# Optimization experiments

Hardware: AMD Instinct MI355X
Metric: run time of the kernel (lower is better)

Reference implementation:

```python
import jax, jax.numpy as jnp
import numpy as np

EMBED_DIM = 1024
NUM_HEADS = 16
HEAD_DIM = EMBED_DIM // NUM_HEADS


def setup_inputs() -> dict:
    key = jax.random.key(0)
    ks = jax.random.split(key, 9)
    B, S, D = 2, 2048, EMBED_DIM
    scale = 1.0 / np.sqrt(D)
    x = jax.random.normal(ks[0], (B, S, D), dtype=jnp.float32)
    # Linear params (torch nn.Linear: y = x @ W.T + b); store W as [out, in]
    Wq = jax.random.normal(ks[1], (D, D), dtype=jnp.float32) * scale
    bq = jnp.zeros((D,), dtype=jnp.float32)
    Wk = jax.random.normal(ks[2], (D, D), dtype=jnp.float32) * scale
    bk = jnp.zeros((D,), dtype=jnp.float32)
    Wv = jax.random.normal(ks[3], (D, D), dtype=jnp.float32) * scale
    bv = jnp.zeros((D,), dtype=jnp.float32)
    Wo = jax.random.normal(ks[4], (D, D), dtype=jnp.float32) * scale
    bo = jnp.zeros((D,), dtype=jnp.float32)
    return {"x": x, "Wq": Wq, "bq": bq, "Wk": Wk, "bk": bk,
            "Wv": Wv, "bv": bv, "Wo": Wo, "bo": bo}


def reference(x, Wq, bq, Wk, bk, Wv, bv, Wo, bo):
    B, S, D = x.shape
    H, Hd = NUM_HEADS, HEAD_DIM
    scaling = Hd ** -0.5
    # projections (torch Linear: x @ W.T + b)
    q = (x @ Wq.T + bq).reshape(B, S, H, Hd).transpose(0, 2, 1, 3)  # [B,H,S,Hd]
    k = (x @ Wk.T + bk).reshape(B, S, H, Hd).transpose(0, 2, 1, 3)
    v = (x @ Wv.T + bv).reshape(B, S, H, Hd).transpose(0, 2, 1, 3)
    # full score matrix, as in the original (no flash tiling)
    scores = jnp.einsum('bhqd,bhkd->bhqk', q, k) * scaling  # [B,H,S,S]
    attn = jax.nn.softmax(scores, axis=-1)
    # dropout is identity in eval mode
    out = jnp.einsum('bhqk,bhkd->bhqd', attn, v)  # [B,H,S,Hd]
    out = out.transpose(0, 2, 1, 3).reshape(B, S, D)
    return out @ Wo.T + bo
```

## Files before the change

kernel.cpp:

```cpp
#include <hip/hip_runtime.h>
#include <stdint.h>

typedef unsigned short u16;
typedef short short8 __attribute__((ext_vector_type(8)));
typedef short bh4 __attribute__((ext_vector_type(4)));
typedef float f32x4 __attribute__((ext_vector_type(4)));

__device__ __forceinline__ u16 f2bf_fast(float f) {
  union { float f; uint32_t u; } x;
  x.f = f;
  return (u16)((x.u + 0x8000u) >> 16);
}

__device__ __forceinline__ uint32_t pack2bf(float lo, float hi) {
  union { float f; uint32_t u; } a, b;
  a.f = lo; b.f = hi;
  return __builtin_amdgcn_perm(b.u + 0x8000u, a.u + 0x8000u, 0x07060302u);
}

__device__ __forceinline__ float bf2f(uint32_t u) {
  union { uint32_t u; float f; } x;
  x.u = u << 16;
  return x.f;
}

__device__ __forceinline__ void gload_lds16(const void* g, void* l) {
  __builtin_amdgcn_global_load_lds(
      (const __attribute__((address_space(1))) void*)g,
      (__attribute__((address_space(3))) void*)l, 16, 0, 0);
}

__device__ __forceinline__ f32x4 mfma16(short8 a, short8 b, f32x4 c) {
  return __builtin_amdgcn_mfma_f32_16x16x32_bf16(a, b, c, 0, 0, 0);
}

__device__ __forceinline__ f32x4 pv_mfma(bh4 a, bh4 b, f32x4 c) {
#if defined(__AMDGCN__) || defined(__HIP_DEVICE_COMPILE__)
  return __builtin_amdgcn_mfma_f32_16x16x16bf16_1k(a, b, c, 0, 0, 0);
#else
  (void)a; (void)b;
  return c;
#endif
}

__device__ __forceinline__ short8 ldfrag(const u16* base, int tile, int kc,
                                         int lane) {
  return *(const short8*)(base + ((((tile << 5) + kc) << 6) + lane) * 8);
}

#define QSCALE 0.18033688011112042f

__global__ void pack_all(const float* __restrict__ x, const float* __restrict__ wq,
                         const float* __restrict__ wk, const float* __restrict__ wv,
                         const float* __restrict__ wo, u16* __restrict__ xp,
                         u16* __restrict__ wp) {
  const int gi = blockIdx.x * 256 + threadIdx.x;
  const int lane = gi & 63;
  const int kc = (gi >> 6) & 31;
  const int rt = gi >> 11;
  const int col = kc * 32 + (lane >> 4) * 8;
  const float* src;
  int row;
  if (rt < 256) {
    src = x;
    row = rt * 16 + (lane & 15);
  } else {
    const int wti = rt - 256;
    const int widx = wti >> 6;
    src = (widx == 0) ? wq : (widx == 1) ? wk : (widx == 2) ? wv : wo;
    row = (wti & 63) * 16 + (lane & 15);
  }
  const float4* p = (const float4*)(src + (size_t)row * 1024 + col);
  const float4 v0 = p[0], v1 = p[1];
  uint4 o;
  o.x = pack2bf(v0.x, v0.y);
  o.y = pack2bf(v0.z, v0.w);
  o.z = pack2bf(v1.x, v1.y);
  o.w = pack2bf(v1.z, v1.w);
  u16* dst = (rt < 256) ? xp : wp;
  const int og = (rt < 256) ? gi : gi - 524288;
  ((uint4*)dst)[og] = o;
}

__global__ __launch_bounds__(256, 3) void proj_qkv(
    const u16* __restrict__ xp, const u16* __restrict__ wp,
    const float* __restrict__ bq, const float* __restrict__ bk,
    const float* __restrict__ bv, u16* __restrict__ qw, u16* __restrict__ kw,
    u16* __restrict__ vw) {
  const int gid = blockIdx.x * 4 + (threadIdx.x >> 6);
  const int lane = threadIdx.x & 63;
  const int quad = lane >> 4, l15 = lane & 15;
  const bool isQK = gid < 2048;
  int at0, bt0, bm, bn;
  const u16 *Ap, *Bp;
  if (isQK) {
    bn = gid >> 6; bm = gid & 63;
    Ap = xp; at0 = bm * 4;
    Bp = wp; bt0 = bn * 4;
  } else {
    const int h = gid - 2048;
    bn = h & 63; bm = h >> 6;
    Ap = wp; at0 = 128 + bm * 4;
    Bp = xp; bt0 = bn * 4;
  }

  f32x4 acc[4][4] = {};
  short8 af[2][4], bf[2][4];
#pragma unroll
  for (int mt = 0; mt < 4; ++mt) af[0][mt] = ldfrag(Ap, at0 + mt, 0, lane);
#pragma unroll
  for (int nt = 0; nt < 4; ++nt) bf[0][nt] = ldfrag(Bp, bt0 + nt, 0, lane);

#pragma unroll 4
  for (int kc = 0; kc < 32; ++kc) {
    const int cur = kc & 1, nxt = cur ^ 1;
    if (kc < 31) {
#pragma unroll
      for (int mt = 0; mt < 4; ++mt)
        af[nxt][mt] = ldfrag(Ap, at0 + mt, kc + 1, lane);
#pragma unroll
      for (int nt = 0; nt < 4; ++nt)
        bf[nxt][nt] = ldfrag(Bp, bt0 + nt, kc + 1, lane);
    }
#pragma unroll
    for (int mt = 0; mt < 4; ++mt)
#pragma unroll
      for (int nt = 0; nt < 4; ++nt)
        acc[mt][nt] = mfma16(af[cur][mt], bf[cur][nt], acc[mt][nt]);
  }

#pragma unroll
  for (int nt = 0; nt < 4; ++nt) {
    const int n = bn * 64 + nt * 16 + l15;
#pragma unroll
    for (int mt = 0; mt < 4; ++mt)
#pragma unroll
      for (int r = 0; r < 4; ++r) {
        const int m = bm * 64 + mt * 16 + quad * 4 + r;
        const float a = acc[mt][nt][r];
        if (isQK) {
          const bool isQ = (bn < 16);
          const int nn = isQ ? n : n - 1024;
          const float v = isQ ? (a + bq[nn]) * QSCALE : a + bk[nn];
          u16* op = isQ ? qw : kw;
          const int b = m >> 11, s = m & 2047, hh = nn >> 6, d = nn & 63;
          op[((size_t)((b * 16 + hh) * 2048 + s)) * 64 + d] = f2bf_fast(v);
        } else {
          const float v = a + bv[m];
          const int b = n >> 11, s = n & 2047;
          vw[((size_t)(b * 1024 + m)) * 2048 + s] = f2bf_fast(v);
        }
      }
  }
}

__global__ __launch_bounds__(256) void attn_kernel(
    const u16* __restrict__ Q, const u16* __restrict__ Kt,
    const u16* __restrict__ Vt, u16* __restrict__ op0, u16* __restrict__ op1,
    float* __restrict__ lp) {
  __shared__ __align__(16) u16 Sm[16384];
  const int tid = threadIdx.x, lane = tid & 63, w = tid >> 6;
  const int quad = lane >> 4, l15 = lane & 15;
  const int qt = blockIdx.x;
  const int bh = blockIdx.y >> 1;
  const int ks = blockIdx.y & 1;

  const char* Qb = (const char*)(Q + ((size_t)bh * 2048 + qt * 128) * 64);
  const char* Kb = (const char*)(Kt + ((size_t)bh * 2048 + ks * 1024) * 64);
  const char* Vb = (const char*)(Vt + (size_t)bh * 64 * 2048 + ks * 1024);

  auto stageKV = [&](int kt, int b) {
    u16* Kl = Sm + b * 4096;
    u16* Vl = Sm + 8192 + b * 4096;
#pragma unroll
    for (int i = 0; i < 2; ++i) {
      const int G = (w * 2 + i) * 64 + lane;
      const int r = G >> 3, sl = G & 7;
      gload_lds16(Kb + (size_t)(kt * 64 + r) * 128 + ((sl ^ (r & 7)) * 16),
                  &Kl[G * 8]);
      gload_lds16(Vb + (size_t)r * 4096 + kt * 128 + ((sl ^ (r & 7)) * 16),
                  &Vl[G * 8]);
    }
  };

#pragma unroll
  for (int i = 0; i < 4; ++i) {
    const int G = (w * 4 + i) * 64 + lane;
    const int row = G >> 3, sl = G & 7;
    u16* qdst = (G < 512) ? (Sm + 4096) : (Sm + 12288);
    gload_lds16(Qb + (size_t)row * 128 + ((sl ^ (row & 7)) * 16),
                &qdst[(G & 511) * 8]);
  }
  stageKV(0, 0);
  __syncthreads();

  const u16* qreg = (w < 2) ? (Sm + 4096) : (Sm + 12288);
  const int qr0 = (w & 1) * 32;
  short8 aq[2][2];
#pragma unroll
  for (int mt = 0; mt < 2; ++mt)
#pragma unroll
    for (int kc = 0; kc < 2; ++kc)
      aq[mt][kc] = *(const short8*)&qreg[(qr0 + mt * 16 + l15) * 64 +
                                         (((kc * 4 + quad) ^ (l15 & 7)) * 8)];
  __syncthreads();

  f32x4 ot[4][2] = {};
  float lsum[2] = {};

  for (int kt = 0; kt < 16; ++kt) {
    const int buf = kt & 1;
    if (kt < 15) stageKV(kt + 1, buf ^ 1);
    const u16* Kl = Sm + buf * 4096;
    const u16* Vl = Sm + 8192 + buf * 4096;

    f32x4 st[2][4] = {};
#pragma unroll
    for (int kc = 0; kc < 2; ++kc)
#pragma unroll
      for (int ntk = 0; ntk < 4; ++ntk) {
        short8 kf = *(const short8*)&Kl[(ntk * 16 + l15) * 64 +
                                        (((kc * 4 + quad) ^ (l15 & 7)) * 8)];
        st[0][ntk] = mfma16(kf, aq[0][kc], st[0][ntk]);
        st[1][ntk] = mfma16(kf, aq[1][kc], st[1][ntk]);
      }

    bh4 bp[2][4];
#pragma unroll
    for (int mt = 0; mt < 2; ++mt)
#pragma unroll
      for (int ntk = 0; ntk < 4; ++ntk) {
        const float e0 = __builtin_amdgcn_exp2f(st[mt][ntk][0]);
        const float e1 = __builtin_amdgcn_exp2f(st[mt][ntk][1]);
        const float e2 = __builtin_amdgcn_exp2f(st[mt][ntk][2]);
        const float e3 = __builtin_amdgcn_exp2f(st[mt][ntk][3]);
        lsum[mt] += (e0 + e1) + (e2 + e3);
        union { uint32_t u[2]; bh4 s; } pb;
        pb.u[0] = pack2bf(e0, e1);
        pb.u[1] = pack2bf(e2, e3);
        bp[mt][ntk] = pb.s;
      }

#pragma unroll
    for (int ntk = 0; ntk < 4; ++ntk) {
      const int swz = ((ntk * 2 + (quad >> 1)) ^ (l15 & 7)) * 8 + (quad & 1) * 4;
#pragma unroll
      for (int ntd = 0; ntd < 4; ++ntd) {
        bh4 vf = *(const bh4*)&Vl[(ntd * 16 + l15) * 64 + swz];
        ot[ntd][0] = pv_mfma(vf, bp[0][ntk], ot[ntd][0]);
        ot[ntd][1] = pv_mfma(vf, bp[1][ntk], ot[ntd][1]);
      }
    }
    if (kt < 15) __syncthreads();
  }

  const int b = bh >> 4, h = bh & 15;
  u16* op = ks ? op1 : op0;
#pragma unroll
  for (int mt = 0; mt < 2; ++mt) {
    float l = lsum[mt];
    l += __shfl_xor(l, 16);
    l += __shfl_xor(l, 32);
    const int srow = qt * 128 + w * 32 + mt * 16 + l15;
    if (quad == 0) lp[((size_t)(ks * 32 + bh)) * 2048 + srow] = l;
    const int rt = b * 128 + qt * 8 + w * 2 + mt;
#pragma unroll
    for (int ntd = 0; ntd < 4; ++ntd) {
      const int kc = h * 2 + (ntd >> 1);
      const int lnq = ((ntd & 1) * 2 + (quad >> 1)) & 3;
      const int j0 = (quad & 1) * 4;
      uint2 ov;
      ov.x = pack2bf(ot[ntd][mt][0], ot[ntd][mt][1]);
      ov.y = pack2bf(ot[ntd][mt][2], ot[ntd][mt][3]);
      *(uint2*)(op + ((size_t)((rt * 32 + kc) * 64 + lnq * 16 + l15)) * 8 + j0) = ov;
    }
  }
}

__global__ void attn_combine(const u16* __restrict__ op0,
                             const u16* __restrict__ op1,
                             const float* __restrict__ lp,
                             u16* __restrict__ awp) {
  const int g = blockIdx.x * 256 + threadIdx.x;
  const int ln = g & 63;
  const int kc = (g >> 6) & 31;
  const int rt = g >> 11;
  const int row = rt * 16 + (ln & 15);
  const int b = row >> 11, s = row & 2047;
  const int h = kc >> 1;
  const int lidx = (b * 16 + h) * 2048 + s;
  const float inv = __builtin_amdgcn_rcpf(lp[lidx] + lp[lidx + 65536]);
  const uint4 a0 = ((const uint4*)op0)[g];
  const uint4 a1 = ((const uint4*)op1)[g];
  uint4 o;
  o.x = pack2bf((bf2f(a0.x) + bf2f(a1.x)) * inv,
                (bf2f(a0.x >> 16) + bf2f(a1.x >> 16)) * inv);
  o.y = pack2bf((bf2f(a0.y) + bf2f(a1.y)) * inv,
                (bf2f(a0.y >> 16) + bf2f(a1.y >> 16)) * inv);
  o.z = pack2bf((bf2f(a0.z) + bf2f(a1.z)) * inv,
                (bf2f(a0.z >> 16) + bf2f(a1.z >> 16)) * inv);
  o.w = pack2bf((bf2f(a0.w) + bf2f(a1.w)) * inv,
                (bf2f(a0.w >> 16) + bf2f(a1.w >> 16)) * inv);
  ((uint4*)awp)[g] = o;
}

__global__ __launch_bounds__(256, 3) void out_proj(const u16* __restrict__ awp,
                                                   const u16* __restrict__ wp,
                                                   const float* __restrict__ bo,
                                                   float* __restrict__ out) {
  const int gid = blockIdx.x * 4 + (threadIdx.x >> 6);
  const int lane = threadIdx.x & 63;
  const int quad = lane >> 4, l15 = lane & 15;
  const int bm = gid & 63, bnn = gid >> 6;
  const int at0 = bm * 4, bt0 = 192 + bnn * 2;

  f32x4 acc[4][2] = {};
  short8 af[2][4], bf[2][2];
#pragma unroll
  for (int mt = 0; mt < 4; ++mt) af[0][mt] = ldfrag(awp, at0 + mt, 0, lane);
#pragma unroll
  for (int nt = 0; nt < 2; ++nt) bf[0][nt] = ldfrag(wp, bt0 + nt, 0, lane);

#pragma unroll 4
  for (int kc = 0; kc < 32; ++kc) {
    const int cur = kc & 1, nxt = cur ^ 1;
    if (kc < 31) {
#pragma unroll
      for (int mt = 0; mt < 4; ++mt)
        af[nxt][mt] = ldfrag(awp, at0 + mt, kc + 1, lane);
#pragma unroll
      for (int nt = 0; nt < 2; ++nt)
        bf[nxt][nt] = ldfrag(wp, bt0 + nt, kc + 1, lane);
    }
#pragma unroll
    for (int mt = 0; mt < 4; ++mt)
#pragma unroll
      for (int nt = 0; nt < 2; ++nt)
        acc[mt][nt] = mfma16(af[cur][mt], bf[cur][nt], acc[mt][nt]);
  }

#pragma unroll
  for (int nt = 0; nt < 2; ++nt) {
    const int n = bnn * 32 + nt * 16 + l15;
    const float bb = bo[n];
#pragma unroll
    for (int mt = 0; mt < 4; ++mt)
#pragma unroll
      for (int r = 0; r < 4; ++r) {
        const int m = bm * 64 + mt * 16 + quad * 4 + r;
        out[(size_t)m * 1024 + n] = acc[mt][nt][r] + bb;
      }
  }
}

extern "C" void kernel_launch(void* const* d_in, const int* in_sizes, int n_in,
                              void* d_out, int out_size, void* d_ws, size_t ws_size,
                              hipStream_t stream) {
  const float* x  = (const float*)d_in[0];
  const float* Wq = (const float*)d_in[1];
  const float* bq = (const float*)d_in[2];
  const float* Wk = (const float*)d_in[3];
  const float* bk = (const float*)d_in[4];
  const float* Wv = (const float*)d_in[5];
  const float* bv = (const float*)d_in[6];
  const float* Wo = (const float*)d_in[7];
  const float* bo = (const float*)d_in[8];

  const size_t M4 = (size_t)4 * 1024 * 1024;
  u16* xp  = (u16*)d_ws;
  u16* wp  = xp + M4;
  u16* qw  = wp + M4;
  u16* kw  = qw + M4;
  u16* vw  = kw + M4;
  u16* op1 = vw + M4;
  u16* awp = op1 + M4;
  float* lp = (float*)(awp + M4);
  u16* op0 = xp;

  pack_all<<<4096, 256, 0, stream>>>(x, Wq, Wk, Wv, Wo, xp, wp);

  proj_qkv<<<768, 256, 0, stream>>>(xp, wp, bq, bk, bv, qw, kw, vw);

  attn_kernel<<<dim3(16, 64), 256, 0, stream>>>(qw, kw, vw, op0, op1, lp);

  attn_combine<<<2048, 256, 0, stream>>>(op0, op1, lp, awp);

  out_proj<<<512, 256, 0, stream>>>(awp, wp, bo, (float*)d_out);
}
```

Measured before the change: 210.9 us.

## Switch attention inner loop to 32x32x16 MFMA with permlane-swapped P fragments

Rewrites the attention kernel's QK^T and PV products to use 32x32x16 bf16 MFMA instead of 16x16x32 and 16x16x16 ones. The exponentiated scores are packed with hardware v_cvt_pk_bf16_f32 and rearranged in registers with v_permlane32_swap, so they feed the PV MFMA directly as 8-wide fragments. The goal is fewer MFMA and LDS fragment-load instructions per tile and cheaper packing. It also sets a launch-bounds occupancy hint of 4 blocks and changes the epilogue layout mapping. The larger accumulators raise register pressure, and any error in the fragment mapping would give wrong results.

```diff
diff --git a/kernel.cpp b/kernel.cpp
--- a/kernel.cpp
+++ b/kernel.cpp
@@ -3,8 +3,9 @@
 
 typedef unsigned short u16;
 typedef short short8 __attribute__((ext_vector_type(8)));
-typedef short bh4 __attribute__((ext_vector_type(4)));
 typedef float f32x4 __attribute__((ext_vector_type(4)));
+typedef float f32x16 __attribute__((ext_vector_type(16)));
+typedef float f32x2 __attribute__((ext_vector_type(2)));
 
 __device__ __forceinline__ u16 f2bf_fast(float f) {
   union { float f; uint32_t u; } x;
@@ -24,6 +25,16 @@
   return x.f;
 }
 
+__device__ __forceinline__ uint32_t cvtpk(float lo, float hi) {
+  uint32_t r;
+  asm("v_cvt_pk_bf16_f32 %0, %1, %2" : "=v"(r) : "v"(lo), "v"(hi));
+  return r;
+}
+
+__device__ __forceinline__ void permswap(uint32_t& a, uint32_t& b) {
+  asm("v_permlane32_swap_b32 %0, %1" : "+v"(a), "+v"(b));
+}
+
 __device__ __forceinline__ void gload_lds16(const void* g, void* l) {
   __builtin_amdgcn_global_load_lds(
       (const __attribute__((address_space(1))) void*)g,
@@ -34,13 +45,8 @@
   return __builtin_amdgcn_mfma_f32_16x16x32_bf16(a, b, c, 0, 0, 0);
 }
 
-__device__ __forceinline__ f32x4 pv_mfma(bh4 a, bh4 b, f32x4 c) {
-#if defined(__AMDGCN__) || defined(__HIP_DEVICE_COMPILE__)
-  return __builtin_amdgcn_mfma_f32_16x16x16bf16_1k(a, b, c, 0, 0, 0);
-#else
-  (void)a; (void)b;
-  return c;
-#endif
+__device__ __forceinline__ f32x16 mfma32(short8 a, short8 b, f32x16 c) {
+  return __builtin_amdgcn_mfma_f32_32x32x16_bf16(a, b, c, 0, 0, 0);
 }
 
 __device__ __forceinline__ short8 ldfrag(const u16* base, int tile, int kc,
@@ -154,13 +160,13 @@
   }
 }
 
-__global__ __launch_bounds__(256) void attn_kernel(
+__global__ __launch_bounds__(256, 4) void attn_kernel(
     const u16* __restrict__ Q, const u16* __restrict__ Kt,
     const u16* __restrict__ Vt, u16* __restrict__ op0, u16* __restrict__ op1,
     float* __restrict__ lp) {
   __shared__ __align__(16) u16 Sm[16384];
   const int tid = threadIdx.x, lane = tid & 63, w = tid >> 6;
-  const int quad = lane >> 4, l15 = lane & 15;
+  const int l31 = lane & 31, hi = lane >> 5, l7 = lane & 7;
   const int qt = blockIdx.x;
   const int bh = blockIdx.y >> 1;
   const int ks = blockIdx.y & 1;
@@ -196,17 +202,14 @@
 
   const u16* qreg = (w < 2) ? (Sm + 4096) : (Sm + 12288);
   const int qr0 = (w & 1) * 32;
-  short8 aq[2][2];
-#pragma unroll
-  for (int mt = 0; mt < 2; ++mt)
-#pragma unroll
-    for (int kc = 0; kc < 2; ++kc)
-      aq[mt][kc] = *(const short8*)&qreg[(qr0 + mt * 16 + l15) * 64 +
-                                         (((kc * 4 + quad) ^ (l15 & 7)) * 8)];
+  short8 aq[4];
+#pragma unroll
+  for (int ds = 0; ds < 4; ++ds)
+    aq[ds] = *(const short8*)&qreg[(qr0 + l31) * 64 + (((ds << 1) + hi) ^ l7) * 8];
   __syncthreads();
 
-  f32x4 ot[4][2] = {};
-  float lsum[2] = {};
+  f32x16 ot[2] = {};
+  f32x2 l2 = {0.f, 0.f};
 
   for (int kt = 0; kt < 16; ++kt) {
     const int buf = kt & 1;
@@ -214,41 +217,41 @@
     const u16* Kl = Sm + buf * 4096;
     const u16* Vl = Sm + 8192 + buf * 4096;
 
-    f32x4 st[2][4] = {};
-#pragma unroll
-    for (int kc = 0; kc < 2; ++kc)
-#pragma unroll
-      for (int ntk = 0; ntk < 4; ++ntk) {
-        short8 kf = *(const short8*)&Kl[(ntk * 16 + l15) * 64 +
-                                        (((kc * 4 + quad) ^ (l15 & 7)) * 8)];
-        st[0][ntk] = mfma16(kf, aq[0][kc], st[0][ntk]);
-        st[1][ntk] = mfma16(kf, aq[1][kc], st[1][ntk]);
+#pragma unroll
+    for (int t = 0; t < 2; ++t) {
+      f32x16 st = {};
+#pragma unroll
+      for (int ds = 0; ds < 4; ++ds) {
+        short8 kf = *(const short8*)&Kl[(t * 32 + l31) * 64 +
+                                        (((ds << 1) + hi) ^ l7) * 8];
+        st = mfma32(kf, aq[ds], st);
       }
-
-    bh4 bp[2][4];
-#pragma unroll
-    for (int mt = 0; mt < 2; ++mt)
-#pragma unroll
-      for (int ntk = 0; ntk < 4; ++ntk) {
-        const float e0 = __builtin_amdgcn_exp2f(st[mt][ntk][0]);
-        const float e1 = __builtin_amdgcn_exp2f(st[mt][ntk][1]);
-        const float e2 = __builtin_amdgcn_exp2f(st[mt][ntk][2]);
-        const float e3 = __builtin_amdgcn_exp2f(st[mt][ntk][3]);
-        lsum[mt] += (e0 + e1) + (e2 + e3);
-        union { uint32_t u[2]; bh4 s; } pb;
-        pb.u[0] = pack2bf(e0, e1);
-        pb.u[1] = pack2bf(e2, e3);
-        bp[mt][ntk] = pb.s;
-      }
-
-#pragma unroll
-    for (int ntk = 0; ntk < 4; ++ntk) {
-      const int swz = ((ntk * 2 + (quad >> 1)) ^ (l15 & 7)) * 8 + (quad & 1) * 4;
-#pragma unroll
-      for (int ntd = 0; ntd < 4; ++ntd) {
-        bh4 vf = *(const bh4*)&Vl[(ntd * 16 + l15) * 64 + swz];
-        ot[ntd][0] = pv_mfma(vf, bp[0][ntk], ot[ntd][0]);
-        ot[ntd][1] = pv_mfma(vf, bp[1][ntk], ot[ntd][1]);
+      float e[16];
+#pragma unroll
+      for (int i = 0; i < 16; ++i) e[i] = __builtin_amdgcn_exp2f(st[i]);
+#pragma unroll
+      for (int i = 0; i < 8; ++i) l2 += (f32x2){e[2 * i], e[2 * i + 1]};
+
+      uint32_t p01 = cvtpk(e[0], e[1]),   p23 = cvtpk(e[2], e[3]);
+      uint32_t p45 = cvtpk(e[4], e[5]),   p67 = cvtpk(e[6], e[7]);
+      uint32_t p89 = cvtpk(e[8], e[9]),   pAB = cvtpk(e[10], e[11]);
+      uint32_t pCD = cvtpk(e[12], e[13]), pEF = cvtpk(e[14], e[15]);
+      permswap(p01, p45);
+      permswap(p23, p67);
+      permswap(p89, pCD);
+      permswap(pAB, pEF);
+      union { uint32_t u[4]; short8 s; } b0, b1;
+      b0.u[0] = p01; b0.u[1] = p23; b0.u[2] = p45; b0.u[3] = p67;
+      b1.u[0] = p89; b1.u[1] = pAB; b1.u[2] = pCD; b1.u[3] = pEF;
+
+#pragma unroll
+      for (int dt = 0; dt < 2; ++dt) {
+#pragma unroll
+        for (int s2 = 0; s2 < 2; ++s2) {
+          short8 vf = *(const short8*)&Vl[(dt * 32 + l31) * 64 +
+                                          ((((t * 2 + s2) << 1) + hi) ^ l7) * 8];
+          ot[dt] = mfma32(vf, s2 ? b1.s : b0.s, ot[dt]);
+        }
       }
     }
     if (kt < 15) __syncthreads();
@@ -256,23 +259,21 @@
 
   const int b = bh >> 4, h = bh & 15;
   u16* op = ks ? op1 : op0;
-#pragma unroll
-  for (int mt = 0; mt < 2; ++mt) {
-    float l = lsum[mt];
-    l += __shfl_xor(l, 16);
-    l += __shfl_xor(l, 32);
-    const int srow = qt * 128 + w * 32 + mt * 16 + l15;
-    if (quad == 0) lp[((size_t)(ks * 32 + bh)) * 2048 + srow] = l;
-    const int rt = b * 128 + qt * 8 + w * 2 + mt;
-#pragma unroll
-    for (int ntd = 0; ntd < 4; ++ntd) {
-      const int kc = h * 2 + (ntd >> 1);
-      const int lnq = ((ntd & 1) * 2 + (quad >> 1)) & 3;
-      const int j0 = (quad & 1) * 4;
+  float l = l2.x + l2.y;
+  l += __shfl_xor(l, 32);
+  const int srow = qt * 128 + w * 32 + l31;
+  if (hi == 0) lp[((size_t)(ks * 32 + bh)) * 2048 + srow] = l;
+  const int rt = b * 128 + qt * 8 + w * 2 + (l31 >> 4);
+#pragma unroll
+  for (int dt = 0; dt < 2; ++dt) {
+    const int kc = h * 2 + dt;
+#pragma unroll
+    for (int g = 0; g < 4; ++g) {
+      const int ln = (lane & 15) + 16 * g;
       uint2 ov;
-      ov.x = pack2bf(ot[ntd][mt][0], ot[ntd][mt][1]);
-      ov.y = pack2bf(ot[ntd][mt][2], ot[ntd][mt][3]);
-      *(uint2*)(op + ((size_t)((rt * 32 + kc) * 64 + lnq * 16 + l15)) * 8 + j0) = ov;
+      ov.x = cvtpk(ot[dt][4 * g + 0], ot[dt][4 * g + 1]);
+      ov.y = cvtpk(ot[dt][4 * g + 2], ot[dt][4 * g + 3]);
+      *(uint2*)(op + ((size_t)((rt * 32 + kc) * 64 + ln)) * 8 + hi * 4) = ov;
     }
   }
 }
```

Result: faster. 199.1 us (-5.6%).
